# Performance work log

Measured on AMD Instinct MI355X. Metric: run time of the kernel, lower is better.

The kernel has to match this reference:

```python
import jax, jax.numpy as jnp
import numpy as np

MARGIN = 1.0
EPS = 1e-8  # torch.cosine_similarity default eps


def _cosine(a, b):
    num = jnp.sum(a * b, axis=1)
    den = jnp.maximum(jnp.linalg.norm(a, axis=1) * jnp.linalg.norm(b, axis=1), EPS)
    return num / den


def setup_inputs() -> dict:
    key = jax.random.key(0)
    k1, k2 = jax.random.split(key)
    B, D = 8192, 512
    anchor = jax.random.normal(k1, (B, D), dtype=jnp.float32)
    positive = jax.random.normal(k2, (B, D), dtype=jnp.float32)
    return {"anchor": anchor, "positive": positive}


def reference(anchor, positive):
    B = positive.shape[0]
    a_n = anchor / jnp.linalg.norm(anchor, axis=1, keepdims=True)
    p_n = positive / jnp.linalg.norm(positive, axis=1, keepdims=True)
    sim = a_n @ p_n.T                      # [B, B] cosine similarity
    mask = 1.0 - jnp.eye(B, dtype=sim.dtype)
    sim = sim * mask                       # zero diagonal
    # margin branch of NegariveSampler (margin=1): abs(sim - margin), zeros -> -inf, argmax
    score = jnp.abs(sim - MARGIN) * mask
    score = jnp.where(score == 0.0, -jnp.inf, score)
    neg_idx = jnp.argmax(score, axis=1)    # [B]
    neg = p_n[neg_idx]                     # gather normalized positives as negatives
    cos_ap = _cosine(anchor, positive)
    cos_an = _cosine(anchor, neg)
    loss = jax.nn.relu(MARGIN + cos_ap - cos_an)
    return loss.mean()
```

## Files before the change

kernel.cpp:

```cpp
#include <hip/hip_runtime.h>
#include <stdint.h>

typedef int   i32x8 __attribute__((ext_vector_type(8)));
typedef float f32x4 __attribute__((ext_vector_type(4)));

#define B_ROWS 8192
#define D_DIM  512

__device__ __forceinline__ uint32_t enc_f32(float f) {
  uint32_t s = __float_as_uint(f);
  return (s & 0x80000000u) ? ~s : (s | 0x80000000u);
}
__device__ __forceinline__ float dec_f32(uint32_t e) {
  uint32_t s = (e & 0x80000000u) ? (e ^ 0x80000000u) : ~e;
  return __uint_as_float(s);
}

__global__ __launch_bounds__(256) void norm_kernel(
    const float* __restrict__ anchor, const float* __restrict__ positive,
    uint32_t* __restrict__ a8, uint32_t* __restrict__ p8,
    float* __restrict__ cos_ap, uint32_t* __restrict__ minenc)
{
  const int wave = threadIdx.x >> 6, lane = threadIdx.x & 63;
  const int r = blockIdx.x * 4 + wave;

  const float4* av = (const float4*)(anchor   + (size_t)r * D_DIM) + lane * 2;
  const float4* pv = (const float4*)(positive + (size_t)r * D_DIM) + lane * 2;
  float4 a0 = av[0], a1 = av[1];
  float4 p0 = pv[0], p1 = pv[1];

  float sa = a0.x*a0.x + a0.y*a0.y + a0.z*a0.z + a0.w*a0.w
           + a1.x*a1.x + a1.y*a1.y + a1.z*a1.z + a1.w*a1.w;
  float sp = p0.x*p0.x + p0.y*p0.y + p0.z*p0.z + p0.w*p0.w
           + p1.x*p1.x + p1.y*p1.y + p1.z*p1.z + p1.w*p1.w;
  float dp = a0.x*p0.x + a0.y*p0.y + a0.z*p0.z + a0.w*p0.w
           + a1.x*p1.x + a1.y*p1.y + a1.z*p1.z + a1.w*p1.w;

#pragma unroll
  for (int d = 1; d < 64; d <<= 1) {
    sa += __shfl_xor(sa, d);
    sp += __shfl_xor(sp, d);
    dp += __shfl_xor(dp, d);
  }

  const float na = sqrtf(sa), np = sqrtf(sp);
  const float ia = 1.0f / na, ip = 1.0f / np;

  float na0 = a0.x*ia, na1 = a0.y*ia, na2 = a0.z*ia, na3 = a0.w*ia;
  float na4 = a1.x*ia, na5 = a1.y*ia, na6 = a1.z*ia, na7 = a1.w*ia;
  float np0 = p0.x*ip, np1 = p0.y*ip, np2 = p0.z*ip, np3 = p0.w*ip;
  float np4 = p1.x*ip, np5 = p1.y*ip, np6 = p1.z*ip, np7 = p1.w*ip;

  uint32_t aw0 = __builtin_amdgcn_cvt_pk_fp8_f32(na0, na1, 0,  false);
  aw0          = __builtin_amdgcn_cvt_pk_fp8_f32(na2, na3, aw0, true);
  uint32_t aw1 = __builtin_amdgcn_cvt_pk_fp8_f32(na4, na5, 0,  false);
  aw1          = __builtin_amdgcn_cvt_pk_fp8_f32(na6, na7, aw1, true);
  uint32_t pw0 = __builtin_amdgcn_cvt_pk_fp8_f32(np0, np1, 0,  false);
  pw0          = __builtin_amdgcn_cvt_pk_fp8_f32(np2, np3, pw0, true);
  uint32_t pw1 = __builtin_amdgcn_cvt_pk_fp8_f32(np4, np5, 0,  false);
  pw1          = __builtin_amdgcn_cvt_pk_fp8_f32(np6, np7, pw1, true);

  ((uint2*)a8)[(size_t)r * 64 + lane] = make_uint2(aw0, aw1);
  ((uint2*)p8)[(size_t)r * 64 + lane] = make_uint2(pw0, pw1);

  if (lane == 0) {
    cos_ap[r] = dp / fmaxf(na * np, 1e-8f);
    minenc[r] = 0xFFFFFFFFu;
  }
}

__device__ __forceinline__ void load16_to_lds(const void* g, void* l) {
  __builtin_amdgcn_global_load_lds(
      (__attribute__((address_space(1))) uint32_t*)(uintptr_t)(g),
      (__attribute__((address_space(3))) uint32_t*)(uintptr_t)(l),
      16, 0, 0);
}

__global__ __launch_bounds__(256, 2) void simmin_kernel(
    const uint8_t* __restrict__ a8, const uint8_t* __restrict__ p8,
    uint32_t* __restrict__ minenc)
{
  __shared__ __attribute__((aligned(16))) uint8_t Alds[2][128 * 128];
  __shared__ __attribute__((aligned(16))) uint8_t Plds[2][128 * 128];
  __shared__ float redmin[256];

  const int tid  = threadIdx.x;
  const int lane = tid & 63;
  const int wave = tid >> 6;
  const int waveM = wave >> 1, waveN = wave & 1;
  const int quad = lane >> 4;
  const int l15  = lane & 15;

  const int bid = blockIdx.x;
  const int blockRow = (bid & 7) * 8 + ((bid >> 3) & 7);
  const int blockCol = bid >> 6;

  f32x4 acc[4][4];
  const f32x4 zero = {0.f, 0.f, 0.f, 0.f};
#pragma unroll
  for (int i = 0; i < 4; i++)
#pragma unroll
    for (int j = 0; j < 4; j++) acc[i][j] = zero;

  const int srow = lane >> 3;
  const int sk   = (lane & 7) ^ srow;
  const uint8_t* aBase = a8 + (size_t)(blockRow * 128) * D_DIM;
  const uint8_t* pBase = p8 + (size_t)(blockCol * 128) * D_DIM;

  auto stage = [&](int k0, int buf) {
#pragma unroll
    for (int c = 0; c < 4; c++) {
      const int chunk = wave * 4 + c;
      const size_t goff = (size_t)(chunk * 8 + srow) * D_DIM + k0 + sk * 16;
      load16_to_lds(aBase + goff, &Alds[buf][chunk * 1024]);
      load16_to_lds(pBase + goff, &Plds[buf][chunk * 1024]);
    }
  };

  stage(0, 0);

#pragma unroll
  for (int k = 0; k < 4; k++) {
    __syncthreads();
    const int buf = k & 1;

    i32x8 af[4], bfr[4];
#pragma unroll
    for (int mf = 0; mf < 4; mf++) {
      const int r = waveM * 64 + mf * 16 + l15;
      const int rx = r & 7;
      const int4 lo = *(const int4*)&Alds[buf][r * 128 + (((quad * 2 + 0) ^ rx) * 16)];
      const int4 hi = *(const int4*)&Alds[buf][r * 128 + (((quad * 2 + 1) ^ rx) * 16)];
      af[mf] = (i32x8){lo.x, lo.y, lo.z, lo.w, hi.x, hi.y, hi.z, hi.w};
    }
#pragma unroll
    for (int nf = 0; nf < 4; nf++) {
      const int r = waveN * 64 + nf * 16 + l15;
      const int rx = r & 7;
      const int4 lo = *(const int4*)&Plds[buf][r * 128 + (((quad * 2 + 0) ^ rx) * 16)];
      const int4 hi = *(const int4*)&Plds[buf][r * 128 + (((quad * 2 + 1) ^ rx) * 16)];
      bfr[nf] = (i32x8){lo.x, lo.y, lo.z, lo.w, hi.x, hi.y, hi.z, hi.w};
    }

    if (k < 3) stage((k + 1) * 128, (k + 1) & 1);

#pragma unroll
    for (int mf = 0; mf < 4; mf++)
#pragma unroll
      for (int nf = 0; nf < 4; nf++)
        acc[mf][nf] = __builtin_amdgcn_mfma_scale_f32_16x16x128_f8f6f4(
            af[mf], bfr[nf], acc[mf][nf],
            0, 0,
            0, 0x7F7F7F7F,
            0, 0x7F7F7F7F);
  }

  const int rowTileBase = blockRow * 128 + waveM * 64;
  const int colTileBase = blockCol * 128 + waveN * 64;

  float rm[4][4];
#pragma unroll
  for (int mf = 0; mf < 4; mf++)
#pragma unroll
    for (int r = 0; r < 4; r++) rm[mf][r] = 3.0e38f;

#pragma unroll
  for (int mf = 0; mf < 4; mf++) {
#pragma unroll
    for (int nf = 0; nf < 4; nf++) {
      const int col = colTileBase + nf * 16 + l15;
#pragma unroll
      for (int r = 0; r < 4; r++) {
        const int row = rowTileBase + mf * 16 + quad * 4 + r;
        const float v = acc[mf][nf][r];
        rm[mf][r] = (row == col) ? rm[mf][r] : fminf(rm[mf][r], v);
      }
    }
  }
#pragma unroll
  for (int d = 1; d < 16; d <<= 1)
#pragma unroll
    for (int mf = 0; mf < 4; mf++)
#pragma unroll
      for (int r = 0; r < 4; r++)
        rm[mf][r] = fminf(rm[mf][r], __shfl_xor(rm[mf][r], d));

  if (l15 == 0) {
#pragma unroll
    for (int mf = 0; mf < 4; mf++)
#pragma unroll
      for (int r = 0; r < 4; r++)
        redmin[waveN * 128 + waveM * 64 + mf * 16 + quad * 4 + r] = rm[mf][r];
  }
  __syncthreads();

  if (tid < 128) {
    const float m = fminf(redmin[tid], redmin[128 + tid]);
    atomicMin(&minenc[blockRow * 128 + tid], enc_f32(m));
  }
}

__global__ __launch_bounds__(1024) void finalize_kernel(
    const uint32_t* __restrict__ minenc, const float* __restrict__ cos_ap,
    float* __restrict__ out)
{
  float sum = 0.0f;
#pragma unroll
  for (int r = threadIdx.x; r < B_ROWS; r += 1024)
    sum += fmaxf(0.0f, 1.0f + cos_ap[r] - dec_f32(minenc[r]));

#pragma unroll
  for (int d = 1; d < 64; d <<= 1) sum += __shfl_xor(sum, d);
  __shared__ float s[16];
  if ((threadIdx.x & 63) == 0) s[threadIdx.x >> 6] = sum;
  __syncthreads();
  if (threadIdx.x < 64) {
    float t = (threadIdx.x < 16) ? s[threadIdx.x] : 0.0f;
#pragma unroll
    for (int d = 1; d < 16; d <<= 1) t += __shfl_xor(t, d);
    if (threadIdx.x == 0) out[0] = t * (1.0f / (float)B_ROWS);
  }
}

extern "C" void kernel_launch(void* const* d_in, const int* in_sizes, int n_in,
                              void* d_out, int out_size, void* d_ws, size_t ws_size,
                              hipStream_t stream) {
  const float* anchor   = (const float*)d_in[0];
  const float* positive = (const float*)d_in[1];

  char* ws = (char*)d_ws;
  uint32_t* a8     = (uint32_t*)(ws);
  uint32_t* p8     = (uint32_t*)(ws + (4ull << 20));
  float*    cos_ap = (float*)(ws + (8ull << 20));
  uint32_t* minenc = (uint32_t*)(ws + (8ull << 20) + (32ull << 10));
  float*    out = (float*)d_out;

  norm_kernel<<<B_ROWS / 4, 256, 0, stream>>>(anchor, positive, a8, p8,
                                              cos_ap, minenc);
  simmin_kernel<<<4096, 256, 0, stream>>>((const uint8_t*)a8,
                                          (const uint8_t*)p8, minenc);
  finalize_kernel<<<1, 1024, 0, stream>>>(minenc, cos_ap, out);
}
```

Before: 124.2 us.

## Use 32x32x64 FP8 MFMA with 128x256 tiles and fuse final reduction

Switches the similarity GEMM from 16x16x128 to 32x32x64 scaled FP8 MFMA and enlarges each block's tile to 128x256. That halves the grid and gives each wave its own 64 columns with 64-byte K slices and a new LDS swizzle. The separate finalize kernel is removed: a completion counter lets the last block compute the mean loss, saving one launch. This trades more accumulator registers and an atomic counter plus fences for better operand reuse and fewer kernel launches.

```diff
diff --git a/kernel.cpp b/kernel.cpp
--- a/kernel.cpp
+++ b/kernel.cpp
@@ -1,11 +1,12 @@
 #include <hip/hip_runtime.h>
 #include <stdint.h>
 
-typedef int   i32x8 __attribute__((ext_vector_type(8)));
-typedef float f32x4 __attribute__((ext_vector_type(4)));
+typedef int   i32x8  __attribute__((ext_vector_type(8)));
+typedef float f32x16 __attribute__((ext_vector_type(16)));
 
 #define B_ROWS 8192
 #define D_DIM  512
+#define GRID_SIMMIN 2048
 
 __device__ __forceinline__ uint32_t enc_f32(float f) {
   uint32_t s = __float_as_uint(f);
@@ -19,7 +20,8 @@
 __global__ __launch_bounds__(256) void norm_kernel(
     const float* __restrict__ anchor, const float* __restrict__ positive,
     uint32_t* __restrict__ a8, uint32_t* __restrict__ p8,
-    float* __restrict__ cos_ap, uint32_t* __restrict__ minenc)
+    float* __restrict__ cos_ap, uint32_t* __restrict__ minenc,
+    uint32_t* __restrict__ donecnt)
 {
   const int wave = threadIdx.x >> 6, lane = threadIdx.x & 63;
   const int r = blockIdx.x * 4 + wave;
@@ -67,6 +69,7 @@
     cos_ap[r] = dp / fmaxf(na * np, 1e-8f);
     minenc[r] = 0xFFFFFFFFu;
   }
+  if (blockIdx.x == 0 && threadIdx.x == 0) *donecnt = 0u;
 }
 
 __device__ __forceinline__ void load16_to_lds(const void* g, void* l) {
@@ -78,147 +81,157 @@
 
 __global__ __launch_bounds__(256, 2) void simmin_kernel(
     const uint8_t* __restrict__ a8, const uint8_t* __restrict__ p8,
-    uint32_t* __restrict__ minenc)
+    uint32_t* __restrict__ minenc, const float* __restrict__ cos_ap,
+    uint32_t* __restrict__ donecnt, float* __restrict__ out)
 {
-  __shared__ __attribute__((aligned(16))) uint8_t Alds[2][128 * 128];
-  __shared__ __attribute__((aligned(16))) uint8_t Plds[2][128 * 128];
-  __shared__ float redmin[256];
+  __shared__ __attribute__((aligned(16))) uint8_t Alds[2][128 * 64];
+  __shared__ __attribute__((aligned(16))) uint8_t Plds[2][256 * 64];
+  __shared__ float redmin[4][128];
+  __shared__ int   isLast;
 
   const int tid  = threadIdx.x;
   const int lane = tid & 63;
   const int wave = tid >> 6;
-  const int waveM = wave >> 1, waveN = wave & 1;
-  const int quad = lane >> 4;
-  const int l15  = lane & 15;
+  const int half = lane >> 5;
+  const int r31  = lane & 31;
 
   const int bid = blockIdx.x;
   const int blockRow = (bid & 7) * 8 + ((bid >> 3) & 7);
   const int blockCol = bid >> 6;
 
-  f32x4 acc[4][4];
-  const f32x4 zero = {0.f, 0.f, 0.f, 0.f};
+  f32x16 acc[4][2];
 #pragma unroll
   for (int i = 0; i < 4; i++)
 #pragma unroll
-    for (int j = 0; j < 4; j++) acc[i][j] = zero;
-
-  const int srow = lane >> 3;
-  const int sk   = (lane & 7) ^ srow;
+    for (int j = 0; j < 2; j++)
+#pragma unroll
+      for (int e = 0; e < 16; e++) acc[i][j][e] = 0.f;
+
   const uint8_t* aBase = a8 + (size_t)(blockRow * 128) * D_DIM;
-  const uint8_t* pBase = p8 + (size_t)(blockCol * 128) * D_DIM;
+  const uint8_t* pBase = p8 + (size_t)(blockCol * 256) * D_DIM;
+
+  const int sRowOff = lane >> 2;
+  const int sSlot   = lane & 3;
 
   auto stage = [&](int k0, int buf) {
 #pragma unroll
+    for (int c = 0; c < 2; c++) {
+      const int g = wave * 2 + c;
+      const int rowL = g * 16 + sRowOff;
+      const int sp = sSlot ^ ((rowL >> 1) & 3);
+      load16_to_lds(aBase + (size_t)rowL * D_DIM + k0 + sp * 16,
+                    &Alds[buf][g * 1024]);
+    }
+#pragma unroll
     for (int c = 0; c < 4; c++) {
-      const int chunk = wave * 4 + c;
-      const size_t goff = (size_t)(chunk * 8 + srow) * D_DIM + k0 + sk * 16;
-      load16_to_lds(aBase + goff, &Alds[buf][chunk * 1024]);
-      load16_to_lds(pBase + goff, &Plds[buf][chunk * 1024]);
+      const int g = wave * 4 + c;
+      const int rowL = g * 16 + sRowOff;
+      const int sp = sSlot ^ ((rowL >> 1) & 3);
+      load16_to_lds(pBase + (size_t)rowL * D_DIM + k0 + sp * 16,
+                    &Plds[buf][g * 1024]);
     }
   };
 
   stage(0, 0);
 
 #pragma unroll
-  for (int k = 0; k < 4; k++) {
+  for (int k = 0; k < 8; k++) {
     __syncthreads();
     const int buf = k & 1;
 
-    i32x8 af[4], bfr[4];
+    i32x8 af[4], bf2[2];
 #pragma unroll
     for (int mf = 0; mf < 4; mf++) {
-      const int r = waveM * 64 + mf * 16 + l15;
-      const int rx = r & 7;
-      const int4 lo = *(const int4*)&Alds[buf][r * 128 + (((quad * 2 + 0) ^ rx) * 16)];
-      const int4 hi = *(const int4*)&Alds[buf][r * 128 + (((quad * 2 + 1) ^ rx) * 16)];
+      const int rowL = mf * 32 + r31;
+      const int f = (rowL >> 1) & 3;
+      const int4 lo = *(const int4*)&Alds[buf][rowL * 64 + (((half*2  ) ^ f) * 16)];
+      const int4 hi = *(const int4*)&Alds[buf][rowL * 64 + (((half*2+1) ^ f) * 16)];
       af[mf] = (i32x8){lo.x, lo.y, lo.z, lo.w, hi.x, hi.y, hi.z, hi.w};
     }
 #pragma unroll
-    for (int nf = 0; nf < 4; nf++) {
-      const int r = waveN * 64 + nf * 16 + l15;
-      const int rx = r & 7;
-      const int4 lo = *(const int4*)&Plds[buf][r * 128 + (((quad * 2 + 0) ^ rx) * 16)];
-      const int4 hi = *(const int4*)&Plds[buf][r * 128 + (((quad * 2 + 1) ^ rx) * 16)];
-      bfr[nf] = (i32x8){lo.x, lo.y, lo.z, lo.w, hi.x, hi.y, hi.z, hi.w};
-    }
-
-    if (k < 3) stage((k + 1) * 128, (k + 1) & 1);
+    for (int nf = 0; nf < 2; nf++) {
+      const int rowL = wave * 64 + nf * 32 + r31;
+      const int f = (rowL >> 1) & 3;
+      const int4 lo = *(const int4*)&Plds[buf][rowL * 64 + (((half*2  ) ^ f) * 16)];
+      const int4 hi = *(const int4*)&Plds[buf][rowL * 64 + (((half*2+1) ^ f) * 16)];
+      bf2[nf] = (i32x8){lo.x, lo.y, lo.z, lo.w, hi.x, hi.y, hi.z, hi.w};
+    }
+
+    if (k < 7) stage((k + 1) * 64, (k + 1) & 1);
 
 #pragma unroll
     for (int mf = 0; mf < 4; mf++)
 #pragma unroll
-      for (int nf = 0; nf < 4; nf++)
-        acc[mf][nf] = __builtin_amdgcn_mfma_scale_f32_16x16x128_f8f6f4(
-            af[mf], bfr[nf], acc[mf][nf],
+      for (int nf = 0; nf < 2; nf++)
+        acc[mf][nf] = __builtin_amdgcn_mfma_scale_f32_32x32x64_f8f6f4(
+            af[mf], bf2[nf], acc[mf][nf],
             0, 0,
             0, 0x7F7F7F7F,
             0, 0x7F7F7F7F);
   }
 
-  const int rowTileBase = blockRow * 128 + waveM * 64;
-  const int colTileBase = blockCol * 128 + waveN * 64;
-
-  float rm[4][4];
+  float rm[4][16];
 #pragma unroll
   for (int mf = 0; mf < 4; mf++)
 #pragma unroll
-    for (int r = 0; r < 4; r++) rm[mf][r] = 3.0e38f;
+    for (int g = 0; g < 16; g++) rm[mf][g] = 3.0e38f;
 
 #pragma unroll
   for (int mf = 0; mf < 4; mf++) {
 #pragma unroll
-    for (int nf = 0; nf < 4; nf++) {
-      const int col = colTileBase + nf * 16 + l15;
-#pragma unroll
-      for (int r = 0; r < 4; r++) {
-        const int row = rowTileBase + mf * 16 + quad * 4 + r;
-        const float v = acc[mf][nf][r];
-        rm[mf][r] = (row == col) ? rm[mf][r] : fminf(rm[mf][r], v);
+    for (int nf = 0; nf < 2; nf++) {
+      const int col = blockCol * 256 + wave * 64 + nf * 32 + r31;
+#pragma unroll
+      for (int g = 0; g < 16; g++) {
+        const int row = blockRow * 128 + mf * 32 + (g & 3) + 8 * (g >> 2) + 4 * half;
+        const float v = acc[mf][nf][g];
+        rm[mf][g] = (row == col) ? rm[mf][g] : fminf(rm[mf][g], v);
       }
     }
   }
 #pragma unroll
-  for (int d = 1; d < 16; d <<= 1)
+  for (int d = 1; d < 32; d <<= 1)
 #pragma unroll
     for (int mf = 0; mf < 4; mf++)
 #pragma unroll
-      for (int r = 0; r < 4; r++)
-        rm[mf][r] = fminf(rm[mf][r], __shfl_xor(rm[mf][r], d));
-
-  if (l15 == 0) {
+      for (int g = 0; g < 16; g++)
+        rm[mf][g] = fminf(rm[mf][g], __shfl_xor(rm[mf][g], d));
+
+  if (r31 == 0) {
 #pragma unroll
     for (int mf = 0; mf < 4; mf++)
 #pragma unroll
-      for (int r = 0; r < 4; r++)
-        redmin[waveN * 128 + waveM * 64 + mf * 16 + quad * 4 + r] = rm[mf][r];
+      for (int g = 0; g < 16; g++)
+        redmin[wave][mf * 32 + (g & 3) + 8 * (g >> 2) + 4 * half] = rm[mf][g];
   }
   __syncthreads();
 
   if (tid < 128) {
-    const float m = fminf(redmin[tid], redmin[128 + tid]);
+    const float m = fminf(fminf(redmin[0][tid], redmin[1][tid]),
+                          fminf(redmin[2][tid], redmin[3][tid]));
     atomicMin(&minenc[blockRow * 128 + tid], enc_f32(m));
   }
-}
-
-__global__ __launch_bounds__(1024) void finalize_kernel(
-    const uint32_t* __restrict__ minenc, const float* __restrict__ cos_ap,
-    float* __restrict__ out)
-{
-  float sum = 0.0f;
-#pragma unroll
-  for (int r = threadIdx.x; r < B_ROWS; r += 1024)
-    sum += fmaxf(0.0f, 1.0f + cos_ap[r] - dec_f32(minenc[r]));
-
-#pragma unroll
-  for (int d = 1; d < 64; d <<= 1) sum += __shfl_xor(sum, d);
-  __shared__ float s[16];
-  if ((threadIdx.x & 63) == 0) s[threadIdx.x >> 6] = sum;
+
+  __threadfence();
   __syncthreads();
-  if (threadIdx.x < 64) {
-    float t = (threadIdx.x < 16) ? s[threadIdx.x] : 0.0f;
-#pragma unroll
-    for (int d = 1; d < 16; d <<= 1) t += __shfl_xor(t, d);
-    if (threadIdx.x == 0) out[0] = t * (1.0f / (float)B_ROWS);
+  if (tid == 0) {
+    const uint32_t old = atomicAdd(donecnt, 1u);
+    isLast = (old == (uint32_t)(GRID_SIMMIN - 1));
+  }
+  __syncthreads();
+  if (isLast) {
+    float sum = 0.0f;
+    for (int r = tid; r < B_ROWS; r += 256) {
+      const uint32_t e = atomicOr(&minenc[r], 0u);
+      sum += fmaxf(0.0f, 1.0f + cos_ap[r] - dec_f32(e));
+    }
+#pragma unroll
+    for (int d = 1; d < 64; d <<= 1) sum += __shfl_xor(sum, d);
+    if ((tid & 63) == 0) redmin[0][tid >> 6] = sum;
+    __syncthreads();
+    if (tid == 0)
+      out[0] = (redmin[0][0] + redmin[0][1] + redmin[0][2] + redmin[0][3])
+               * (1.0f / (float)B_ROWS);
   }
 }
 
@@ -229,15 +242,16 @@
   const float* positive = (const float*)d_in[1];
 
   char* ws = (char*)d_ws;
-  uint32_t* a8     = (uint32_t*)(ws);
-  uint32_t* p8     = (uint32_t*)(ws + (4ull << 20));
-  float*    cos_ap = (float*)(ws + (8ull << 20));
-  uint32_t* minenc = (uint32_t*)(ws + (8ull << 20) + (32ull << 10));
+  uint32_t* a8      = (uint32_t*)(ws);
+  uint32_t* p8      = (uint32_t*)(ws + (4ull << 20));
+  float*    cos_ap  = (float*)(ws + (8ull << 20));
+  uint32_t* minenc  = (uint32_t*)(ws + (8ull << 20) + (32ull << 10));
+  uint32_t* donecnt = (uint32_t*)(ws + (8ull << 20) + (64ull << 10));
   float*    out = (float*)d_out;
 
   norm_kernel<<<B_ROWS / 4, 256, 0, stream>>>(anchor, positive, a8, p8,
-                                              cos_ap, minenc);
-  simmin_kernel<<<4096, 256, 0, stream>>>((const uint8_t*)a8,
-                                          (const uint8_t*)p8, minenc);
-  finalize_kernel<<<1, 1024, 0, stream>>>(minenc, cos_ap, out);
-}
+                                              cos_ap, minenc, donecnt);
+  simmin_kernel<<<GRID_SIMMIN, 256, 0, stream>>>((const uint8_t*)a8,
+                                                 (const uint8_t*)p8, minenc,
+                                                 cos_ap, donecnt, out);
+}
```

Result: slower. 252.8 us (+103.5%).
